# Kernel tuning notes

Hardware: AMD Instinct MI355X
Metric: run time of the kernel (lower is better)

The kernel has to match this reference:

```python
import jax, jax.numpy as jnp
import numpy as np

B, T, D = 4, 2048, 2048
H = 16
Q_RANK, KV_RANK = 1536, 512
NOPE, ROPE_D, V_D = 128, 64, 128
QK_D = NOPE + ROPE_D  # 192
D_FF = 8192
EPS = 1e-6
THETA = 10000.0
SCALE = QK_D ** -0.5  # mscale = 1 (no rope_scaling)


def _w(key, shape):
    fan_in = shape[0]
    return jax.random.normal(key, shape, dtype=jnp.float32) / np.sqrt(fan_in)


def setup_inputs() -> dict:
    key = jax.random.key(0)
    ks = jax.random.split(key, 16)
    return {
        "x": jax.random.normal(ks[0], (B, T, D), dtype=jnp.float32),
        "ln1_w": jnp.ones((D,), jnp.float32),
        "wq_a": _w(ks[1], (D, Q_RANK)),
        "q_a_ln_w": jnp.ones((Q_RANK,), jnp.float32),
        "wq_b": _w(ks[2], (Q_RANK, H * QK_D)),
        "wkv_a": _w(ks[3], (D, KV_RANK + ROPE_D)),
        "kv_a_ln_w": jnp.ones((KV_RANK,), jnp.float32),
        "wkv_b": _w(ks[4], (KV_RANK, H * (NOPE + V_D))),
        "wo": _w(ks[5], (H * V_D, D)),
        "ln2_w": jnp.ones((D,), jnp.float32),
        "w_gate": _w(ks[6], (D, D_FF)),
        "w_up": _w(ks[7], (D, D_FF)),
        "w_down": _w(ks[8], (D_FF, D)),
        "attention_mask": jnp.ones((B, T), jnp.int32),
        "positions": jnp.broadcast_to(jnp.arange(T, dtype=jnp.int32), (B, T)),
    }


def rmsnorm(x, w):
    return x * jax.lax.rsqrt(jnp.mean(x * x, axis=-1, keepdims=True) + EPS) * w


def apply_rope(x, positions):
    # x: [B, T, h, d], positions: [B, T]
    d = x.shape[-1]
    inv_freq = 1.0 / (THETA ** (jnp.arange(0, d, 2, dtype=jnp.float32) / d))
    ang = positions.astype(jnp.float32)[:, :, None] * inv_freq  # [B,T,d/2]
    cos = jnp.cos(ang)[:, :, None, :]
    sin = jnp.sin(ang)[:, :, None, :]
    x1, x2 = jnp.split(x, 2, axis=-1)
    return jnp.concatenate([x1 * cos - x2 * sin, x2 * cos + x1 * sin], axis=-1)


def reference(x, ln1_w, wq_a, q_a_ln_w, wq_b, wkv_a, kv_a_ln_w, wkv_b, wo,
              ln2_w, w_gate, w_up, w_down, attention_mask, positions):
    # --- MLA attention block ---
    h = rmsnorm(x, ln1_w)
    # low-rank q projection
    q = rmsnorm(h @ wq_a, q_a_ln_w) @ wq_b            # [B,T,H*192]
    q = q.reshape(B, T, H, QK_D)
    q_pass, q_rot = jnp.split(q, [NOPE], axis=-1)
    # compressed kv + shared rope key
    ckv = h @ wkv_a                                    # [B,T,512+64]
    k_c, k_rot = jnp.split(ckv, [KV_RANK], axis=-1)
    k_rot = k_rot.reshape(B, T, 1, ROPE_D)
    kv = rmsnorm(k_c, kv_a_ln_w) @ wkv_b               # [B,T,H*(128+128)]
    kv = kv.reshape(B, T, H, NOPE + V_D)
    k_pass, v = jnp.split(kv, [NOPE], axis=-1)
    # split RoPE on rope dims only
    q_rot = apply_rope(q_rot, positions)
    k_rot = jnp.broadcast_to(apply_rope(k_rot, positions), (B, T, H, ROPE_D))
    qh = jnp.concatenate([q_pass, q_rot], axis=-1)     # [B,T,H,192]
    kh = jnp.concatenate([k_pass, k_rot], axis=-1)     # [B,T,H,192]
    # attention with causal + padding mask (V pad-to-192 then slice is a no-op mathematically)
    scores = jnp.einsum('bqhd,bkhd->bhqk', qh, kh) * SCALE
    causal = jnp.tril(jnp.ones((T, T), bool))
    mask = causal[None, None] & attention_mask[:, None, None, :].astype(bool)
    scores = jnp.where(mask, scores, jnp.finfo(scores.dtype).min)
    attn = jax.nn.softmax(scores, axis=-1)
    o = jnp.einsum('bhqk,bkhd->bqhd', attn, v).reshape(B, T, H * V_D)
    x = x + o @ wo
    # --- MLP block ---
    h2 = rmsnorm(x, ln2_w)
    mlp = (jax.nn.silu(h2 @ w_gate) * (h2 @ w_up)) @ w_down
    return x + mlp
```

## Files before the change

### kernel.cpp

```cpp
#include <hip/hip_runtime.h>

typedef float f32x4 __attribute__((ext_vector_type(4)));
typedef __bf16 bf16x8 __attribute__((ext_vector_type(8)));
typedef unsigned short u16x8 __attribute__((ext_vector_type(8)));
typedef unsigned short u16x4 __attribute__((ext_vector_type(4)));

static __device__ __forceinline__ unsigned short f2b(float f) {
  union { float f; unsigned u; } v; v.f = f;
  unsigned r = v.u + 0x7fffu + ((v.u >> 16) & 1u);
  return (unsigned short)(r >> 16);
}
static __device__ __forceinline__ float b2f(unsigned short s) {
  union { unsigned u; float f; } v; v.u = ((unsigned)s) << 16;
  return v.f;
}
static __device__ __forceinline__ void gload_lds16(const unsigned short* g, unsigned short* l) {
  __builtin_amdgcn_global_load_lds((const __attribute__((address_space(1))) void*)g,
                                   (__attribute__((address_space(3))) void*)l, 16, 0, 0);
}

#define NEG_BIG -3.0e38f

__global__ __launch_bounds__(256) void fill_sentinel(float* __restrict__ out, int n, float v) {
  int i = blockIdx.x * 256 + threadIdx.x;
  if (i < n) out[i] = v;
}

__global__ __launch_bounds__(256) void transpose_convert(const float* __restrict__ in,
                                                         unsigned short* __restrict__ out,
                                                         int K, int N, int in_ld, int row0, int col0,
                                                         float scale) {
  __shared__ float tile[32][33];
  const int k0 = blockIdx.y * 32, n0 = blockIdx.x * 32;
  const int tx = threadIdx.x & 31, ty = threadIdx.x >> 5;
#pragma unroll
  for (int i = 0; i < 32; i += 8) {
    int k = k0 + ty + i, n = n0 + tx;
    tile[ty + i][tx] = (k < K && n < N) ? in[(size_t)(row0 + k) * in_ld + col0 + n] : 0.f;
  }
  __syncthreads();
#pragma unroll
  for (int i = 0; i < 32; i += 8) {
    int n = n0 + ty + i, k = k0 + tx;
    if (n < N && k < K) out[(size_t)n * K + k] = f2b(tile[tx][ty + i] * scale);
  }
}

__global__ __launch_bounds__(256) void rmsnorm_kernel(const float* __restrict__ in,
                                                      const float* __restrict__ w,
                                                      unsigned short* __restrict__ out,
                                                      int ncols, int in_stride, int out_stride) {
  const int row = blockIdx.x;
  const float* rp = in + (size_t)row * in_stride;
  const int n4 = ncols >> 2;
  float4 v[2];
  int nv = 0;
  float ss = 0.f;
  for (int c = threadIdx.x; c < n4; c += 256) {
    float4 xv = reinterpret_cast<const float4*>(rp)[c];
    v[nv++] = xv;
    ss += xv.x * xv.x + xv.y * xv.y + xv.z * xv.z + xv.w * xv.w;
  }
#pragma unroll
  for (int m = 32; m; m >>= 1) ss += __shfl_xor(ss, m);
  __shared__ float red[4];
  if ((threadIdx.x & 63) == 0) red[threadIdx.x >> 6] = ss;
  __syncthreads();
  const float total = red[0] + red[1] + red[2] + red[3];
  const float scale = rsqrtf(total / (float)ncols + 1e-6f);
  nv = 0;
  unsigned short* op = out + (size_t)row * out_stride;
  for (int c = threadIdx.x; c < n4; c += 256) {
    float4 xv = v[nv++];
    float4 wv = reinterpret_cast<const float4*>(w)[c];
    u16x4 o;
    o[0] = f2b(xv.x * scale * wv.x);
    o[1] = f2b(xv.y * scale * wv.y);
    o[2] = f2b(xv.z * scale * wv.z);
    o[3] = f2b(xv.w * scale * wv.w);
    reinterpret_cast<u16x4*>(op)[c] = o;
  }
}

template <int EPI>
__global__ __launch_bounds__(256) void gemm_bt(const unsigned short* __restrict__ A,
                                               const unsigned short* __restrict__ Bt,
                                               float* __restrict__ outf,
                                               unsigned short* __restrict__ outb,
                                               const float* __restrict__ res,
                                               const unsigned short* __restrict__ aux,
                                               int M, int N, int K) {
  __shared__ __align__(16) unsigned short As[128 * 32];
  __shared__ __align__(16) unsigned short Bs[128 * 32];
  const int tid = threadIdx.x;
  const int l = tid & 63;
  const int lr = l & 15, lg = l >> 4;
  const int wr = tid >> 7, wc = (tid >> 6) & 1;

  const int gx = gridDim.x;
  const int nwg = gx * gridDim.y;
  int lin = blockIdx.y * gx + blockIdx.x;
  {
    const int qq = nwg >> 3, rr = nwg & 7;
    const int xcd = lin & 7, idx = lin >> 3;
    lin = (xcd < rr ? xcd * (qq + 1) : rr * (qq + 1) + (xcd - rr) * qq) + idx;
  }
  const int m0 = (lin / gx) * 128, n0 = (lin % gx) * 128;

  f32x4 acc[4][4] = {};

  for (int k0 = 0; k0 < K; k0 += 32) {
#pragma unroll
    for (int j = 0; j < 2; ++j) {
      const int chunk = j * 256 + tid;
      const int row = chunk >> 2, kc = chunk & 3;
      const unsigned short* ga = A + (size_t)(m0 + row) * K + k0 + kc * 8;
      gload_lds16(ga, &As[(size_t)(j * 256 + (tid & 192)) * 8]);
      int rb = n0 + row;
      if (rb > N - 1) rb = N - 1;
      const unsigned short* gb = Bt + (size_t)rb * K + k0 + kc * 8;
      gload_lds16(gb, &Bs[(size_t)(j * 256 + (tid & 192)) * 8]);
    }
    __syncthreads();
    bf16x8 af[4], bfr[4];
#pragma unroll
    for (int mi = 0; mi < 4; ++mi)
      af[mi] = *reinterpret_cast<const bf16x8*>(&As[(wr * 64 + mi * 16 + lr) * 32 + lg * 8]);
#pragma unroll
    for (int ni = 0; ni < 4; ++ni)
      bfr[ni] = *reinterpret_cast<const bf16x8*>(&Bs[(wc * 64 + ni * 16 + lr) * 32 + lg * 8]);
#pragma unroll
    for (int mi = 0; mi < 4; ++mi)
#pragma unroll
      for (int ni = 0; ni < 4; ++ni)
        acc[mi][ni] = __builtin_amdgcn_mfma_f32_16x16x32_bf16(af[mi], bfr[ni], acc[mi][ni], 0, 0, 0);
    __syncthreads();
  }

#pragma unroll
  for (int mi = 0; mi < 4; ++mi) {
#pragma unroll
    for (int ni = 0; ni < 4; ++ni) {
      const int r0 = m0 + wr * 64 + mi * 16 + lg * 4;
      const int c = n0 + wc * 64 + ni * 16 + lr;
      if (c < N) {
#pragma unroll
        for (int j = 0; j < 4; ++j) {
          const size_t idx = (size_t)(r0 + j) * N + c;
          const float v = acc[mi][ni][j];
          if constexpr (EPI == 0) outf[idx] = v;
          else if constexpr (EPI == 1) outb[idx] = f2b(v);
          else if constexpr (EPI == 2) outf[idx] = v + res[idx];
          else if constexpr (EPI == 3) outb[idx] = f2b(v / (1.f + __expf(-v)));
          else outb[idx] = f2b(v * b2f(aux[idx]));
        }
      }
    }
  }
}

template <int EPI>
__global__ __launch_bounds__(512, 1) void gemm256(const unsigned short* __restrict__ A,
                                                  const unsigned short* __restrict__ Bt,
                                                  float* __restrict__ outf,
                                                  unsigned short* __restrict__ outb,
                                                  const float* __restrict__ res,
                                                  const unsigned short* __restrict__ aux,
                                                  int M, int N, int K) {
  __shared__ __align__(16) unsigned short Lds[2][2][2][8192];
  const int tid = threadIdx.x;
  const int l = tid & 63, lr = l & 15, lg = l >> 4;
  const int w = tid >> 6, wr = w >> 2, wn = w & 3;

  const int gn = N >> 8;
  int lin = blockIdx.x;
  {
    const int nwg = gridDim.x;
    lin = (lin & 7) * (nwg >> 3) + (lin >> 3);
  }
  const int npg = gn << 3;
  const int gid = lin / npg;
  const int idx = lin - gid * npg;
  const int m0 = (gid * 8 + (idx & 7)) * 256;
  const int n0 = (idx >> 3) * 256;

  const int NT = K >> 6;
  const int swz = (lg ^ ((lr >> 1) & 3)) * 8;

  f32x4 acc[8][4] = {};

  auto stageh = [&](int mat, int kh, int t) {
    const unsigned short* src = mat ? Bt : A;
    const int rb = mat ? n0 : m0;
    const int d = t & 1;
#pragma unroll
    for (int g = 0; g < 2; ++g) {
      const int c = g * 512 + tid;
      const int row = c >> 2;
      const int kc = (c & 3) ^ ((row >> 1) & 3);
      gload_lds16(src + (size_t)(rb + row) * K + t * 64 + kh * 32 + kc * 8,
                  &Lds[d][mat][kh][(size_t)(g * 512 + (tid & ~63)) * 8]);
    }
  };

  stageh(1, 0, 0); stageh(0, 0, 0); stageh(1, 1, 0); stageh(0, 1, 0);
  if (NT > 1) {
    stageh(1, 0, 1); stageh(0, 0, 1); stageh(1, 1, 1);
    asm volatile("s_waitcnt vmcnt(10)" ::: "memory");
  } else {
    asm volatile("s_waitcnt vmcnt(4)" ::: "memory");
  }
  __builtin_amdgcn_s_barrier();
  __builtin_amdgcn_sched_barrier(0);

#define RD_A(mh, kk, i)                                                                    \
  af[i] = *reinterpret_cast<const bf16x8*>(                                                \
      &Lds[d][0][kk][(wr * 128 + ((mh) * 4 + (i)) * 16 + lr) * 32 + swz])
#define RD_B(kk, ni)                                                                       \
  bfv[ni] = *reinterpret_cast<const bf16x8*>(                                              \
      &Lds[d][1][kk][(wn * 64 + (ni) * 16 + lr) * 32 + swz])
#define MFMA16(mh)                                                                         \
  _Pragma("unroll") for (int i = 0; i < 4; ++i)                                            \
  _Pragma("unroll") for (int ni = 0; ni < 4; ++ni)                                         \
      acc[(mh) * 4 + i][ni] =                                                              \
          __builtin_amdgcn_mfma_f32_16x16x32_bf16(af[i], bfv[ni], acc[(mh) * 4 + i][ni], 0, 0, 0)

  for (int T = 0; T < NT; ++T) {
    const int d = T & 1;
    bf16x8 af[4], bfv[4];

    RD_A(0, 0, 0); RD_A(0, 0, 1); RD_A(0, 0, 2); RD_A(0, 0, 3);
    RD_B(0, 0); RD_B(0, 1); RD_B(0, 2); RD_B(0, 3);
    if (T + 1 < NT) stageh(0, 1, T + 1);
    __builtin_amdgcn_s_setprio(1);
    MFMA16(0);
    __builtin_amdgcn_s_setprio(0);
    __builtin_amdgcn_s_barrier();
    __builtin_amdgcn_sched_barrier(0);

    RD_A(1, 0, 0); RD_A(1, 0, 1); RD_A(1, 0, 2); RD_A(1, 0, 3);
    if (T + 2 < NT) stageh(1, 0, T + 2);
    __builtin_amdgcn_s_setprio(1);
    MFMA16(1);
    __builtin_amdgcn_s_setprio(0);
    if (T + 2 < NT)      asm volatile("s_waitcnt vmcnt(10)" ::: "memory");
    else if (T + 1 < NT) asm volatile("s_waitcnt vmcnt(8)" ::: "memory");
    else                 asm volatile("s_waitcnt vmcnt(0)" ::: "memory");
    __builtin_amdgcn_s_barrier();
    __builtin_amdgcn_sched_barrier(0);

    RD_A(0, 1, 0); RD_A(0, 1, 1); RD_A(0, 1, 2); RD_A(0, 1, 3);
    RD_B(1, 0); RD_B(1, 1); RD_B(1, 2); RD_B(1, 3);
    if (T + 2 < NT) stageh(0, 0, T + 2);
    __builtin_amdgcn_s_setprio(1);
    MFMA16(0);
    __builtin_amdgcn_s_setprio(0);
    __builtin_amdgcn_s_barrier();
    __builtin_amdgcn_sched_barrier(0);

    RD_A(1, 1, 0); RD_A(1, 1, 1); RD_A(1, 1, 2); RD_A(1, 1, 3);
    if (T + 2 < NT) stageh(1, 1, T + 2);
    __builtin_amdgcn_s_setprio(1);
    MFMA16(1);
    __builtin_amdgcn_s_setprio(0);
    if (T + 2 < NT)      asm volatile("s_waitcnt vmcnt(10)" ::: "memory");
    else if (T + 1 < NT) asm volatile("s_waitcnt vmcnt(4)" ::: "memory");
    __builtin_amdgcn_s_barrier();
    __builtin_amdgcn_sched_barrier(0);
  }

#undef RD_A
#undef RD_B
#undef MFMA16

#pragma unroll
  for (int mi = 0; mi < 8; ++mi) {
#pragma unroll
    for (int ni = 0; ni < 4; ++ni) {
      const int r = m0 + wr * 128 + mi * 16 + lg * 4;
      const int c = n0 + wn * 64 + ni * 16 + lr;
#pragma unroll
      for (int j = 0; j < 4; ++j) {
        const size_t idx2 = (size_t)(r + j) * N + c;
        const float v = acc[mi][ni][j];
        if constexpr (EPI == 0) outf[idx2] = v;
        else if constexpr (EPI == 1) outb[idx2] = f2b(v);
        else if constexpr (EPI == 2) outf[idx2] = v + res[idx2];
        else if constexpr (EPI == 3) outb[idx2] = f2b(v / (1.f + __expf(-v)));
        else outb[idx2] = f2b(v * b2f(aux[idx2]));
      }
    }
  }
}

__global__ __launch_bounds__(256) void rope_q(unsigned short* __restrict__ q,
                                              const int* __restrict__ positions) {
  const int row = blockIdx.x;
  const int pos = positions[row];
  unsigned short* qp = q + (size_t)row * 3072;
  const int tid = threadIdx.x;
#pragma unroll
  for (int i = 0; i < 2; ++i) {
    int e = i * 256 + tid;
    int hh = e >> 5, j = e & 31;
    int base = hh * 192 + 128;
    float x1 = b2f(qp[base + j]), x2 = b2f(qp[base + 32 + j]);
    float freq = __expf(-(float)j * (9.210340371976184f / 32.f));
    float sa, ca;
    __sincosf((float)pos * freq, &sa, &ca);
    qp[base + j] = f2b(x1 * ca - x2 * sa);
    qp[base + 32 + j] = f2b(x2 * ca + x1 * sa);
  }
}

__global__ __launch_bounds__(256) void repack_k(const unsigned short* __restrict__ kv,
                                                const float* __restrict__ ckv,
                                                const int* __restrict__ positions,
                                                unsigned short* __restrict__ kh) {
  const int row = blockIdx.x;
  const int tid = threadIdx.x;
  {
    const int hh = tid >> 4, db = tid & 15;
    u16x8 v = *reinterpret_cast<const u16x8*>(kv + (size_t)row * 4096 + hh * 256 + db * 8);
    *reinterpret_cast<u16x8*>(kh + (size_t)row * 3072 + hh * 192 + db * 8) = v;
  }
  __shared__ float o1[32], o2[32];
  if (tid < 32) {
    const int j = tid;
    float x1 = ckv[(size_t)row * 576 + 512 + j];
    float x2 = ckv[(size_t)row * 576 + 544 + j];
    const int pos = positions[row];
    float freq = __expf(-(float)j * (9.210340371976184f / 32.f));
    float sa, ca;
    __sincosf((float)pos * freq, &sa, &ca);
    o1[j] = x1 * ca - x2 * sa;
    o2[j] = x2 * ca + x1 * sa;
  }
  __syncthreads();
#pragma unroll
  for (int i = 0; i < 4; ++i) {
    int e = i * 256 + tid;
    int hh = e >> 6, d = e & 63;
    float v = (d < 32) ? o1[d] : o2[d - 32];
    kh[(size_t)row * 3072 + hh * 192 + 128 + d] = f2b(v);
  }
}

__global__ __launch_bounds__(512) void mla_attn(const unsigned short* __restrict__ qh,
                                                const unsigned short* __restrict__ kh,
                                                const unsigned short* __restrict__ kv,
                                                unsigned short* __restrict__ o) {
  const int T = 2048, H = 16;
  const int bx = blockIdx.x;
  const int b = blockIdx.y >> 4;
  const int h = blockIdx.y & 15;
  const int tid = threadIdx.x, w = tid >> 6, l = tid & 63;
  const int lg = l >> 4, lr = l & 15;

  __shared__ __align__(16) unsigned short Ks[64 * 200];
  __shared__ __align__(16) unsigned short Vts[128 * 64];
  __shared__ __align__(16) unsigned short Pl[8][16 * 72];
  __shared__ float exs[8][16];

  int krow[3], kcol[3];
#pragma unroll
  for (int i = 0; i < 3; ++i) { int c = i * 512 + tid; krow[i] = c / 24; kcol[i] = (c % 24) * 8; }
  const int vkvp = tid >> 4;
  const int vf0 = (tid & 15) * 8;

  const unsigned short* kbase0 = kh + (((size_t)b * T) * H + h) * 192;
  const unsigned short* vbase0 = kv + (((size_t)b * T) * H + h) * 256 + 128;

  bf16x8 ones;
#pragma unroll
  for (int e = 0; e < 8; ++e) ones[e] = (__bf16)1.0f;

  for (int half = 0; half < 2; ++half) {
    const int qt = half ? (15 - bx) : bx;

    bf16x8 qa[6];
    {
      const size_t qrow = (size_t)b * T + qt * 128 + w * 16 + lr;
      const unsigned short* qp = qh + (qrow * H + h) * 192 + lg * 8;
#pragma unroll
      for (int kc = 0; kc < 6; ++kc)
        qa[kc] = *reinterpret_cast<const bf16x8*>(qp + kc * 32);
    }

    u16x8 kreg[3], vregA, vregB;
#pragma unroll
    for (int i = 0; i < 3; ++i)
      kreg[i] = *reinterpret_cast<const u16x8*>(kbase0 + (size_t)krow[i] * 3072 + kcol[i]);
    vregA = *reinterpret_cast<const u16x8*>(vbase0 + (size_t)(2 * vkvp) * 4096 + vf0);
    vregB = *reinterpret_cast<const u16x8*>(vbase0 + (size_t)(2 * vkvp + 1) * 4096 + vf0);

    f32x4 ot[8] = {};
    f32x4 lacc = {};
    float mrow[4] = {NEG_BIG, NEG_BIG, NEG_BIG, NEG_BIG};

    const int ktmax = 2 * qt + 1;
    for (int kt = 0; kt <= ktmax; ++kt) {
#pragma unroll
      for (int i = 0; i < 3; ++i)
        *reinterpret_cast<u16x8*>(&Ks[krow[i] * 200 + kcol[i]]) = kreg[i];
      {
        const int c7 = (vf0 >> 3) & 7;
#pragma unroll
        for (int e = 0; e < 8; ++e) {
          const int blk = (vkvp >> 2) ^ (e ^ c7);
          const unsigned val = (unsigned)(unsigned short)vregA[e] |
                               ((unsigned)(unsigned short)vregB[e] << 16);
          *reinterpret_cast<unsigned*>(&Vts[(vf0 + e) * 64 + blk * 8 + (vkvp & 3) * 2]) = val;
        }
      }
      __syncthreads();

      if (kt < ktmax) {
        const unsigned short* kb = kbase0 + (size_t)(kt + 1) * 64 * 3072;
        const unsigned short* vb = vbase0 + (size_t)(kt + 1) * 64 * 4096;
#pragma unroll
        for (int i = 0; i < 3; ++i)
          kreg[i] = *reinterpret_cast<const u16x8*>(kb + (size_t)krow[i] * 3072 + kcol[i]);
        vregA = *reinterpret_cast<const u16x8*>(vb + (size_t)(2 * vkvp) * 4096 + vf0);
        vregB = *reinterpret_cast<const u16x8*>(vb + (size_t)(2 * vkvp + 1) * 4096 + vf0);
      }

      f32x4 s4[4];
#pragma unroll
      for (int ni = 0; ni < 4; ++ni) {
        f32x4 a = {};
#pragma unroll
        for (int kc = 0; kc < 6; ++kc) {
          bf16x8 kf = *reinterpret_cast<const bf16x8*>(&Ks[(ni * 16 + lr) * 200 + kc * 32 + lg * 8]);
          a = __builtin_amdgcn_mfma_f32_16x16x32_bf16(qa[kc], kf, a, 0, 0, 0);
        }
        s4[ni] = a;
      }
      if (kt >= 2 * qt) {
#pragma unroll
        for (int ni = 0; ni < 4; ++ni) {
          const int colr = ni * 16 + lr;
#pragma unroll
          for (int j = 0; j < 4; ++j) {
            const int qrl = qt * 128 + w * 16 + lg * 4 + j - kt * 64;
            if (colr > qrl) s4[ni][j] = NEG_BIG;
          }
        }
      }

      float pmj[4];
      int need = 0;
#pragma unroll
      for (int j = 0; j < 4; ++j) {
        pmj[j] = fmaxf(fmaxf(s4[0][j], s4[1][j]), fmaxf(s4[2][j], s4[3][j]));
        need |= (pmj[j] > mrow[j] + 8.f) ? 1 : 0;
      }
      if (__any(need)) {
        float al[4];
#pragma unroll
        for (int j = 0; j < 4; ++j) {
          float rm = pmj[j];
#pragma unroll
          for (int m = 1; m < 16; m <<= 1) rm = fmaxf(rm, __shfl_xor(rm, m));
          const float mn = fmaxf(mrow[j], rm);
          al[j] = __expf(mrow[j] - mn);
          mrow[j] = mn;
        }
        if (lr == 0) {
#pragma unroll
          for (int j = 0; j < 4; ++j) exs[w][lg * 4 + j] = al[j];
        }
        const float af = exs[w][lr];
#pragma unroll
        for (int mi = 0; mi < 8; ++mi) {
          ot[mi][0] *= af; ot[mi][1] *= af; ot[mi][2] *= af; ot[mi][3] *= af;
        }
        lacc[0] *= af; lacc[1] *= af; lacc[2] *= af; lacc[3] *= af;
      }

#pragma unroll
      for (int ni = 0; ni < 4; ++ni)
#pragma unroll
        for (int j = 0; j < 4; ++j)
          Pl[w][(lg * 4 + j) * 72 + ni * 16 + lr] = f2b(__expf(s4[ni][j] - mrow[j]));

      bf16x8 pf0 = *reinterpret_cast<const bf16x8*>(&Pl[w][lr * 72 + lg * 8]);
      bf16x8 pf1 = *reinterpret_cast<const bf16x8*>(&Pl[w][lr * 72 + 32 + lg * 8]);
      lacc = __builtin_amdgcn_mfma_f32_16x16x32_bf16(ones, pf0, lacc, 0, 0, 0);
      lacc = __builtin_amdgcn_mfma_f32_16x16x32_bf16(ones, pf1, lacc, 0, 0, 0);
#pragma unroll
      for (int mi = 0; mi < 8; ++mi) {
        const int f = mi * 16 + lr;
        const int sfz = (f & 7) ^ ((f >> 3) & 7);
        const int blk0 = lg ^ sfz;
        const int blk1 = (4 + lg) ^ sfz;
        bf16x8 vf0r = *reinterpret_cast<const bf16x8*>(&Vts[f * 64 + blk0 * 8]);
        ot[mi] = __builtin_amdgcn_mfma_f32_16x16x32_bf16(vf0r, pf0, ot[mi], 0, 0, 0);
        bf16x8 vf1r = *reinterpret_cast<const bf16x8*>(&Vts[f * 64 + blk1 * 8]);
        ot[mi] = __builtin_amdgcn_mfma_f32_16x16x32_bf16(vf1r, pf1, ot[mi], 0, 0, 0);
      }
      __syncthreads();
    }

    const float li = 1.f / lacc[0];
    const size_t orow = (size_t)b * T + qt * 128 + w * 16 + lr;
#pragma unroll
    for (int mi = 0; mi < 8; ++mi)
#pragma unroll
      for (int j = 0; j < 4; ++j) {
        const int feat = mi * 16 + lg * 4 + j;
        o[orow * 2048 + h * 128 + feat] = f2b(ot[mi][j] * li);
      }
  }
}

extern "C" void kernel_launch(void* const* d_in, const int* in_sizes, int n_in,
                              void* d_out, int out_size, void* d_ws, size_t ws_size,
                              hipStream_t stream) {
  (void)in_sizes; (void)n_in;
  const float* x      = (const float*)d_in[0];
  const float* ln1_w  = (const float*)d_in[1];
  const float* wq_a   = (const float*)d_in[2];
  const float* qaln_w = (const float*)d_in[3];
  const float* wq_b   = (const float*)d_in[4];
  const float* wkv_a  = (const float*)d_in[5];
  const float* kvln_w = (const float*)d_in[6];
  const float* wkv_b  = (const float*)d_in[7];
  const float* wo     = (const float*)d_in[8];
  const float* ln2_w  = (const float*)d_in[9];
  const float* w_gate = (const float*)d_in[10];
  const float* w_up   = (const float*)d_in[11];
  const float* w_down = (const float*)d_in[12];
  const int*   pos    = (const int*)d_in[14];
  float* out = (float*)d_out;

  const int Mt = 8192;

  char* ws = (char*)d_ws;
  const size_t R1 = 0;
  const size_t R2 = R1 + 67108864;
  const size_t R3 = R2 + 50331648;
  const size_t R4 = R3 + 50331648;
  const size_t R5 = R4 + 33554432;
  const size_t R6 = R5 + 18874368;
  const size_t REQ = R6 + 9437184;

  if (ws_size < REQ) {
    fill_sentinel<<<dim3((out_size + 255) / 256), dim3(256), 0, stream>>>(
        out, out_size, (float)(ws_size >> 20));
    return;
  }

  float*          qa_f  = (float*)(ws + R1);
  unsigned short* kvbuf = (unsigned short*)(ws + R1);
  unsigned short* qbuf  = (unsigned short*)(ws + R2);
  unsigned short* qan   = (unsigned short*)(ws + R3);
  unsigned short* ckvn  = (unsigned short*)(ws + R3);
  unsigned short* khbuf = (unsigned short*)(ws + R3);
  unsigned short* hbuf  = (unsigned short*)(ws + R4);
  unsigned short* obuf  = (unsigned short*)(ws + R4);
  float*          ckv   = (float*)(ws + R5);
  unsigned short* slotW = (unsigned short*)(ws + R6);
  unsigned short* actb  = (unsigned short*)(ws + 0);
  unsigned short* h2b   = (unsigned short*)(ws + 134217728);
  unsigned short* wsl2  = (unsigned short*)(ws + 167772160);

  dim3 blk(256);
  dim3 blk5(512);
  auto tcf = [&](const float* W, int K, int N, float scale) {
    transpose_convert<<<dim3((N + 31) / 32, (K + 31) / 32), blk, 0, stream>>>(W, slotW, K, N, N, 0, 0, scale);
  };
  auto g256 = [&](auto epi, const unsigned short* Aa, const unsigned short* Bb, float* of,
                  unsigned short* ob, const float* rs, const unsigned short* ax, int N, int K) {
    gemm256<decltype(epi)::value><<<dim3(32 * (N >> 8)), blk5, 0, stream>>>(Aa, Bb, of, ob, rs, ax, Mt, N, K);
  };

  rmsnorm_kernel<<<Mt, blk, 0, stream>>>(x, ln1_w, hbuf, 2048, 2048, 2048);
  tcf(wq_a, 2048, 1536, 1.0f);
  g256(std::integral_constant<int,0>{}, hbuf, slotW, qa_f, nullptr, nullptr, nullptr, 1536, 2048);
  rmsnorm_kernel<<<Mt, blk, 0, stream>>>(qa_f, qaln_w, qan, 1536, 1536, 1536);
  tcf(wq_b, 1536, 3072, 0.07216878364870322f);
  g256(std::integral_constant<int,1>{}, qan, slotW, nullptr, qbuf, nullptr, nullptr, 3072, 1536);
  tcf(wkv_a, 2048, 576, 1.0f);
  gemm_bt<0><<<dim3(5, 64), blk, 0, stream>>>(hbuf, slotW, ckv, nullptr, nullptr, nullptr, Mt, 576, 2048);
  rmsnorm_kernel<<<Mt, blk, 0, stream>>>(ckv, kvln_w, ckvn, 512, 576, 512);
  tcf(wkv_b, 512, 4096, 1.0f);
  g256(std::integral_constant<int,1>{}, ckvn, slotW, nullptr, kvbuf, nullptr, nullptr, 4096, 512);
  rope_q<<<Mt, blk, 0, stream>>>(qbuf, pos);
  repack_k<<<Mt, blk, 0, stream>>>(kvbuf, ckv, pos, khbuf);
  mla_attn<<<dim3(8, 64), blk5, 0, stream>>>(qbuf, khbuf, kvbuf, obuf);
  tcf(wo, 2048, 2048, 1.0f);
  g256(std::integral_constant<int,2>{}, obuf, slotW, out, nullptr, x, nullptr, 2048, 2048);
  rmsnorm_kernel<<<Mt, blk, 0, stream>>>(out, ln2_w, h2b, 2048, 2048, 2048);
  transpose_convert<<<dim3(256, 64), blk, 0, stream>>>(w_gate, wsl2, 2048, 8192, 8192, 0, 0, 1.0f);
  g256(std::integral_constant<int,3>{}, h2b, wsl2, nullptr, actb, nullptr, nullptr, 8192, 2048);
  transpose_convert<<<dim3(256, 64), blk, 0, stream>>>(w_up, wsl2, 2048, 8192, 8192, 0, 0, 1.0f);
  g256(std::integral_constant<int,4>{}, h2b, wsl2, nullptr, actb, nullptr, actb, 8192, 2048);
  transpose_convert<<<dim3(64, 256), blk, 0, stream>>>(w_down, wsl2, 8192, 2048, 2048, 0, 0, 1.0f);
  g256(std::integral_constant<int,2>{}, actb, wsl2, out, nullptr, out, nullptr, 2048, 8192);
}
```

Measured before the change: 1.522 ms.

## Switch gemm256 to 32x32x16 MFMA with two-phase pipeline and new LDS swizzle

Rewrites the main 256x256 GEMM inner loop to use 32x32x16 bf16 MFMA tiles instead of 16x16x32. This cuts the number of LDS fragment reads per MFMA and reduces instruction issue overhead. The four-phase per-k-tile schedule becomes two phases, each staging A and B halves together, with vmcnt waits adjusted to match. The LDS XOR swizzle and the epilogue index mapping change to fit the 32x32 accumulator layout, which risks bank conflicts or wrong wait counts if misaligned.

```diff
diff --git a/kernel.cpp b/kernel.cpp
--- a/kernel.cpp
+++ b/kernel.cpp
@@ -1,6 +1,7 @@
 #include <hip/hip_runtime.h>
 
 typedef float f32x4 __attribute__((ext_vector_type(4)));
+typedef float f32x16 __attribute__((ext_vector_type(16)));
 typedef __bf16 bf16x8 __attribute__((ext_vector_type(8)));
 typedef unsigned short u16x8 __attribute__((ext_vector_type(8)));
 typedef unsigned short u16x4 __attribute__((ext_vector_type(4)));
@@ -169,7 +170,8 @@
                                                   int M, int N, int K) {
   __shared__ __align__(16) unsigned short Lds[2][2][2][8192];
   const int tid = threadIdx.x;
-  const int l = tid & 63, lr = l & 15, lg = l >> 4;
+  const int l = tid & 63;
+  const int l31 = l & 31, l5 = l >> 5, l3 = l & 3;
   const int w = tid >> 6, wr = w >> 2, wn = w & 3;
 
   const int gn = N >> 8;
@@ -185,104 +187,86 @@
   const int n0 = (idx >> 3) * 256;
 
   const int NT = K >> 6;
-  const int swz = (lg ^ ((lr >> 1) & 3)) * 8;
-
-  f32x4 acc[8][4] = {};
+  const int ck0 = ((l5) ^ l3) * 8;
+  const int ck1 = ((2 + l5) ^ l3) * 8;
+
+  f32x16 acc[4][2] = {};
 
   auto stageh = [&](int mat, int kh, int t) {
     const unsigned short* src = mat ? Bt : A;
     const int rb = mat ? n0 : m0;
-    const int d = t & 1;
+    const int dd = t & 1;
 #pragma unroll
     for (int g = 0; g < 2; ++g) {
       const int c = g * 512 + tid;
       const int row = c >> 2;
-      const int kc = (c & 3) ^ ((row >> 1) & 3);
+      const int kc = (c & 3) ^ (row & 3);
       gload_lds16(src + (size_t)(rb + row) * K + t * 64 + kh * 32 + kc * 8,
-                  &Lds[d][mat][kh][(size_t)(g * 512 + (tid & ~63)) * 8]);
+                  &Lds[dd][mat][kh][(size_t)(g * 512 + (tid & ~63)) * 8]);
     }
   };
 
-  stageh(1, 0, 0); stageh(0, 0, 0); stageh(1, 1, 0); stageh(0, 1, 0);
-  if (NT > 1) {
-    stageh(1, 0, 1); stageh(0, 0, 1); stageh(1, 1, 1);
-    asm volatile("s_waitcnt vmcnt(10)" ::: "memory");
-  } else {
-    asm volatile("s_waitcnt vmcnt(4)" ::: "memory");
-  }
+  stageh(0, 0, 0); stageh(1, 0, 0);
+  stageh(0, 1, 0); stageh(1, 1, 0);
+  stageh(0, 0, 1); stageh(1, 0, 1);
+  asm volatile("s_waitcnt vmcnt(8)" ::: "memory");
   __builtin_amdgcn_s_barrier();
   __builtin_amdgcn_sched_barrier(0);
 
-#define RD_A(mh, kk, i)                                                                    \
-  af[i] = *reinterpret_cast<const bf16x8*>(                                                \
-      &Lds[d][0][kk][(wr * 128 + ((mh) * 4 + (i)) * 16 + lr) * 32 + swz])
-#define RD_B(kk, ni)                                                                       \
-  bfv[ni] = *reinterpret_cast<const bf16x8*>(                                              \
-      &Lds[d][1][kk][(wn * 64 + (ni) * 16 + lr) * 32 + swz])
-#define MFMA16(mh)                                                                         \
-  _Pragma("unroll") for (int i = 0; i < 4; ++i)                                            \
-  _Pragma("unroll") for (int ni = 0; ni < 4; ++ni)                                         \
-      acc[(mh) * 4 + i][ni] =                                                              \
-          __builtin_amdgcn_mfma_f32_16x16x32_bf16(af[i], bfv[ni], acc[(mh) * 4 + i][ni], 0, 0, 0)
+#define GPHASE(kh, STAGE_STMT, WAIT_STMT)                                                   \
+  {                                                                                         \
+    bf16x8 afr[8], bfr[4];                                                                  \
+    _Pragma("unroll") for (int rg = 0; rg < 4; ++rg) {                                      \
+      afr[rg * 2 + 0] = *reinterpret_cast<const bf16x8*>(                                   \
+          &Lds[d][0][kh][(wr * 128 + rg * 32 + l31) * 32 + ck0]);                           \
+      afr[rg * 2 + 1] = *reinterpret_cast<const bf16x8*>(                                   \
+          &Lds[d][0][kh][(wr * 128 + rg * 32 + l31) * 32 + ck1]);                           \
+    }                                                                                       \
+    _Pragma("unroll") for (int cg = 0; cg < 2; ++cg) {                                      \
+      bfr[cg * 2 + 0] = *reinterpret_cast<const bf16x8*>(                                   \
+          &Lds[d][1][kh][(wn * 64 + cg * 32 + l31) * 32 + ck0]);                            \
+      bfr[cg * 2 + 1] = *reinterpret_cast<const bf16x8*>(                                   \
+          &Lds[d][1][kh][(wn * 64 + cg * 32 + l31) * 32 + ck1]);                            \
+    }                                                                                       \
+    STAGE_STMT                                                                              \
+    __builtin_amdgcn_s_setprio(1);                                                          \
+    _Pragma("unroll") for (int rg = 0; rg < 4; ++rg)                                        \
+    _Pragma("unroll") for (int cg = 0; cg < 2; ++cg) {                                      \
+      acc[rg][cg] = __builtin_amdgcn_mfma_f32_32x32x16_bf16(afr[rg * 2 + 0], bfr[cg * 2 + 0], \
+                                                            acc[rg][cg], 0, 0, 0);          \
+      acc[rg][cg] = __builtin_amdgcn_mfma_f32_32x32x16_bf16(afr[rg * 2 + 1], bfr[cg * 2 + 1], \
+                                                            acc[rg][cg], 0, 0, 0);          \
+    }                                                                                       \
+    __builtin_amdgcn_s_setprio(0);                                                          \
+    WAIT_STMT                                                                               \
+    __builtin_amdgcn_s_barrier();                                                           \
+    __builtin_amdgcn_sched_barrier(0);                                                      \
+  }
 
   for (int T = 0; T < NT; ++T) {
     const int d = T & 1;
-    bf16x8 af[4], bfv[4];
-
-    RD_A(0, 0, 0); RD_A(0, 0, 1); RD_A(0, 0, 2); RD_A(0, 0, 3);
-    RD_B(0, 0); RD_B(0, 1); RD_B(0, 2); RD_B(0, 3);
-    if (T + 1 < NT) stageh(0, 1, T + 1);
-    __builtin_amdgcn_s_setprio(1);
-    MFMA16(0);
-    __builtin_amdgcn_s_setprio(0);
-    __builtin_amdgcn_s_barrier();
-    __builtin_amdgcn_sched_barrier(0);
-
-    RD_A(1, 0, 0); RD_A(1, 0, 1); RD_A(1, 0, 2); RD_A(1, 0, 3);
-    if (T + 2 < NT) stageh(1, 0, T + 2);
-    __builtin_amdgcn_s_setprio(1);
-    MFMA16(1);
-    __builtin_amdgcn_s_setprio(0);
-    if (T + 2 < NT)      asm volatile("s_waitcnt vmcnt(10)" ::: "memory");
-    else if (T + 1 < NT) asm volatile("s_waitcnt vmcnt(8)" ::: "memory");
-    else                 asm volatile("s_waitcnt vmcnt(0)" ::: "memory");
-    __builtin_amdgcn_s_barrier();
-    __builtin_amdgcn_sched_barrier(0);
-
-    RD_A(0, 1, 0); RD_A(0, 1, 1); RD_A(0, 1, 2); RD_A(0, 1, 3);
-    RD_B(1, 0); RD_B(1, 1); RD_B(1, 2); RD_B(1, 3);
-    if (T + 2 < NT) stageh(0, 0, T + 2);
-    __builtin_amdgcn_s_setprio(1);
-    MFMA16(0);
-    __builtin_amdgcn_s_setprio(0);
-    __builtin_amdgcn_s_barrier();
-    __builtin_amdgcn_sched_barrier(0);
-
-    RD_A(1, 1, 0); RD_A(1, 1, 1); RD_A(1, 1, 2); RD_A(1, 1, 3);
-    if (T + 2 < NT) stageh(1, 1, T + 2);
-    __builtin_amdgcn_s_setprio(1);
-    MFMA16(1);
-    __builtin_amdgcn_s_setprio(0);
-    if (T + 2 < NT)      asm volatile("s_waitcnt vmcnt(10)" ::: "memory");
-    else if (T + 1 < NT) asm volatile("s_waitcnt vmcnt(4)" ::: "memory");
-    __builtin_amdgcn_s_barrier();
-    __builtin_amdgcn_sched_barrier(0);
-  }
-
-#undef RD_A
-#undef RD_B
-#undef MFMA16
-
-#pragma unroll
-  for (int mi = 0; mi < 8; ++mi) {
-#pragma unroll
-    for (int ni = 0; ni < 4; ++ni) {
-      const int r = m0 + wr * 128 + mi * 16 + lg * 4;
-      const int c = n0 + wn * 64 + ni * 16 + lr;
-#pragma unroll
-      for (int j = 0; j < 4; ++j) {
-        const size_t idx2 = (size_t)(r + j) * N + c;
-        const float v = acc[mi][ni][j];
+    GPHASE(0,
+      { if (T + 1 < NT) { stageh(0, 1, T + 1); stageh(1, 1, T + 1); } },
+      { if (T + 1 < NT) asm volatile("s_waitcnt vmcnt(8)" ::: "memory");
+        else            asm volatile("s_waitcnt vmcnt(0)" ::: "memory"); });
+    GPHASE(1,
+      { if (T + 2 < NT) { stageh(0, 0, T + 2); stageh(1, 0, T + 2); } },
+      { if (T + 2 < NT)      asm volatile("s_waitcnt vmcnt(8)" ::: "memory");
+        else if (T + 1 < NT) asm volatile("s_waitcnt vmcnt(4)" ::: "memory"); });
+  }
+#undef GPHASE
+
+#pragma unroll
+  for (int rg = 0; rg < 4; ++rg) {
+#pragma unroll
+    for (int cg = 0; cg < 2; ++cg) {
+      const int c = n0 + wn * 64 + cg * 32 + l31;
+      const int rbase = m0 + wr * 128 + rg * 32 + 4 * l5;
+#pragma unroll
+      for (int reg = 0; reg < 16; ++reg) {
+        const int r = rbase + (reg & 3) + 8 * (reg >> 2);
+        const size_t idx2 = (size_t)r * N + c;
+        const float v = acc[rg][cg][reg];
         if constexpr (EPI == 0) outf[idx2] = v;
         else if constexpr (EPI == 1) outb[idx2] = f2b(v);
         else if constexpr (EPI == 2) outf[idx2] = v + res[idx2];
```

Result: slower. 1.703 ms (+11.9%).
